# Performance work log

Hardware: AMD Instinct MI355X
Metric: run time of the kernel (lower is better)

The kernel has to match this reference:

```python
import jax, jax.numpy as jnp
import numpy as np

N_NODES = 50000
N_EDGES = 800000
D_FEAT = 64
N_OUT = 64
N_LAYERS = 2


def setup_inputs() -> dict:
    key = jax.random.key(0)
    ks = jax.random.split(key, 6)
    x = jax.random.normal(ks[0], (N_NODES, D_FEAT), dtype=jnp.float32)
    rows = jnp.sort(jax.random.randint(ks[1], (N_EDGES,), 0, N_NODES, dtype=jnp.int32))
    cols = jax.random.randint(ks[2], (N_EDGES,), 0, N_NODES, dtype=jnp.int32)
    vals = jax.random.uniform(ks[3], (N_EDGES,), dtype=jnp.float32)
    scalars = jnp.ones((N_LAYERS,), dtype=jnp.float32)  # per-layer scalar param (init ones)
    W = jax.random.normal(ks[4], (N_OUT, D_FEAT), dtype=jnp.float32) / np.sqrt(D_FEAT)
    b = jnp.zeros((N_OUT,), dtype=jnp.float32)
    return {"x": x, "rows": rows, "cols": cols, "vals": vals,
            "scalars": scalars, "W": W, "b": b}


def _spmm(rows, cols, vals, x):
    # y[r] = sum_e vals[e] * x[cols[e]]  (sparse adj in COO)
    msgs = vals[:, None] * x[cols]  # [E, D] gather + scale
    return jax.ops.segment_sum(msgs, rows, num_segments=N_NODES,
                               indices_are_sorted=True)


def reference(x, rows, cols, vals, scalars, W, b):
    # ScalarGCNNoFeatureTrans forward (dropout in eval mode = identity)
    h = x
    for l in range(N_LAYERS):
        h = jax.nn.elu(_spmm(rows, cols, vals, scalars[l] * h))
    return h @ W.T + b
```

## Files before the change

kernel.cpp:

```cpp
#include <hip/hip_runtime.h>
#include <hip/hip_fp16.h>
#include <math.h>

#define N_NODES 50000
#define N_EDGES 800000
#define D_FEAT 64
#define XCHUNKS (N_NODES * D_FEAT / 8)
#define NBLK 3125
#define ECAP 512

__device__ __forceinline__ unsigned pack2h(float a, float b) {
    __half2 h = __floats2half2_rn(a, b);
    return *reinterpret_cast<unsigned*>(&h);
}
__device__ __forceinline__ __half2 as_h2(unsigned u) {
    return *reinterpret_cast<__half2*>(&u);
}

__device__ __forceinline__ float elu_f(float x) {
    return x > 0.f ? x : (__expf(x) - 1.f);
}

__global__ __launch_bounds__(256) void prep_kernel(const int* __restrict__ rows,
                                                   const float* __restrict__ x,
                                                   int* __restrict__ row_ptr,
                                                   unsigned short* __restrict__ xhf) {
    const int i = blockIdx.x * blockDim.x + threadIdx.x;
    if (i <= N_NODES) {
        int lo = 0, hi = N_EDGES;
        while (lo < hi) {
            int mid = (lo + hi) >> 1;
            if (rows[mid] < i) lo = mid + 1; else hi = mid;
        }
        row_ptr[i] = lo;
    }
    if (i < XCHUNKS) {
        const float4 f0 = *reinterpret_cast<const float4*>(x + (size_t)i * 8);
        const float4 f1 = *reinterpret_cast<const float4*>(x + (size_t)i * 8 + 4);
        uint4 w;
        w.x = pack2h(f0.x, f0.y);
        w.y = pack2h(f0.z, f0.w);
        w.z = pack2h(f1.x, f1.y);
        w.w = pack2h(f1.z, f1.w);
        *reinterpret_cast<uint4*>(xhf + (size_t)i * 8) = w;
    }
}

template <bool MASKED>
__device__ __forceinline__ void edge_step8_lds(const char* __restrict__ hb,
                                               const int2* __restrict__ elds,
                                               int le, int le1, int boff,
                                               __half2& A0, __half2& A1,
                                               __half2& B0, __half2& B1) {
    int off[8]; unsigned v2[8];
    #pragma unroll
    for (int k = 0; k < 8; ++k) {
        const int t = le + k;
        const int idx = MASKED ? (t < le1 ? t : le1 - 1) : t;
        const int2 p = elds[idx];
        off[k] = p.x;
        v2[k]  = (unsigned)p.y;
        if (MASKED) v2[k] = (t < le1) ? v2[k] : 0u;
    }
    uint2 gg[8];
    #pragma unroll
    for (int k = 0; k < 8; ++k)
        gg[k] = *reinterpret_cast<const uint2*>(hb + (unsigned)(off[k] + boff));
    #pragma unroll
    for (int k = 0; k < 8; ++k) {
        const __half2 vv = as_h2(v2[k]);
        if (k & 1) {
            B0 = __hfma2(vv, as_h2(gg[k].x), B0);
            B1 = __hfma2(vv, as_h2(gg[k].y), B1);
        } else {
            A0 = __hfma2(vv, as_h2(gg[k].x), A0);
            A1 = __hfma2(vv, as_h2(gg[k].y), A1);
        }
    }
}

template <bool FUSE>
__global__ __launch_bounds__(256) void gcn_layer(
    const unsigned short* __restrict__ h_in,
    const int*   __restrict__ cols,
    const float* __restrict__ vals,
    const int*   __restrict__ row_ptr,
    const float* __restrict__ scalar_p,
    const float* __restrict__ W,
    const float* __restrict__ bvec,
    void*        __restrict__ h_out)
{
    __shared__ int2     elds[ECAP];
    __shared__ unsigned Wh[FUSE ? 64 * 33 : 1];
    __shared__ float    ylds[FUSE ? 4 * 4 * 68 : 1];

    const int tid  = threadIdx.x;
    const int lane = tid & 63;
    const int wave = tid >> 6;
    const int g    = lane >> 4;
    const int f4   = lane & 15;
    const int boff = f4 * 8;

    const int rb  = blockIdx.x * 16;
    const int eb0 = row_ptr[rb];
    const int eb1 = row_ptr[rb + 16];
    const int cnt = min(eb1 - eb0, ECAP);
    for (int i = tid; i < cnt; i += 256) {
        const int   c = cols[eb0 + i];
        const float v = vals[eb0 + i];
        elds[i] = make_int2(c << 7, (int)pack2h(v, v));
    }
    if constexpr (FUSE) {
        for (int i = tid; i < 64 * 32; i += 256) {
            const int j = i >> 5, c = i & 31;
            Wh[j * 33 + c] = pack2h(W[j * 64 + 2 * c], W[j * 64 + 2 * c + 1]);
        }
    }
    __syncthreads();

    const int row = rb + wave * 4 + g;
    const float s  = scalar_p[0];
    const int  e0  = row_ptr[row];
    const int  e1  = row_ptr[row + 1];
    const char* hb = (const char*)h_in;

    __half2 A0 = __floats2half2_rn(0.f, 0.f);
    __half2 A1 = A0, B0 = A0, B1 = A0;

    const int ecap = eb0 + cnt;
    const int le0 = e0 - eb0;
    const int le1 = (e1 < ecap ? e1 : ecap) - eb0;
    int le = le0;
    for (; le + 8 <= le1; le += 8)
        edge_step8_lds<false>(hb, elds, le, le1, boff, A0, A1, B0, B1);
    if (le < le1)
        edge_step8_lds<true>(hb, elds, le, le1, boff, A0, A1, B0, B1);
    for (int e = (e0 > ecap ? e0 : ecap); e < e1; ++e) {
        const int   c = cols[e];
        const float v = vals[e];
        const __half2 vv = as_h2(pack2h(v, v));
        const uint2 gg = *reinterpret_cast<const uint2*>(hb + (unsigned)((c << 7) + boff));
        A0 = __hfma2(vv, as_h2(gg.x), A0);
        A1 = __hfma2(vv, as_h2(gg.y), A1);
    }

    const float2 a0 = __half22float2(A0), a1 = __half22float2(A1);
    const float2 b0 = __half22float2(B0), b1 = __half22float2(B1);
    float4 acc;
    acc.x = elu_f((a0.x + b0.x) * s);
    acc.y = elu_f((a0.y + b0.y) * s);
    acc.z = elu_f((a1.x + b1.x) * s);
    acc.w = elu_f((a1.y + b1.y) * s);

    if constexpr (!FUSE) {
        uint2 wv;
        wv.x = pack2h(acc.x, acc.y);
        wv.y = pack2h(acc.z, acc.w);
        *reinterpret_cast<uint2*>((char*)h_out + (size_t)row * 128 + boff) = wv;
    } else {
        float* yw = ylds + wave * (4 * 68);
        *reinterpret_cast<float4*>(yw + g * 68 + f4 * 4) = acc;
        asm volatile("s_waitcnt lgkmcnt(0)" ::: "memory");

        const int j = lane;
        const float bj = bvec[j];
        float o0 = bj, o1 = bj, o2 = bj, o3 = bj;
        #pragma unroll
        for (int d0 = 0; d0 < 16; ++d0) {
            const float2 wA = __half22float2(as_h2(Wh[j * 33 + 2 * d0]));
            const float2 wB = __half22float2(as_h2(Wh[j * 33 + 2 * d0 + 1]));
            const float4 y0 = *reinterpret_cast<const float4*>(yw + 0 * 68 + d0 * 4);
            const float4 y1 = *reinterpret_cast<const float4*>(yw + 1 * 68 + d0 * 4);
            const float4 y2 = *reinterpret_cast<const float4*>(yw + 2 * 68 + d0 * 4);
            const float4 y3 = *reinterpret_cast<const float4*>(yw + 3 * 68 + d0 * 4);
            o0 = fmaf(y0.x, wA.x, o0); o0 = fmaf(y0.y, wA.y, o0);
            o0 = fmaf(y0.z, wB.x, o0); o0 = fmaf(y0.w, wB.y, o0);
            o1 = fmaf(y1.x, wA.x, o1); o1 = fmaf(y1.y, wA.y, o1);
            o1 = fmaf(y1.z, wB.x, o1); o1 = fmaf(y1.w, wB.y, o1);
            o2 = fmaf(y2.x, wA.x, o2); o2 = fmaf(y2.y, wA.y, o2);
            o2 = fmaf(y2.z, wB.x, o2); o2 = fmaf(y2.w, wB.y, o2);
            o3 = fmaf(y3.x, wA.x, o3); o3 = fmaf(y3.y, wA.y, o3);
            o3 = fmaf(y3.z, wB.x, o3); o3 = fmaf(y3.w, wB.y, o3);
        }
        const size_t rbase = (size_t)(rb + wave * 4) * D_FEAT;
        float* outp = (float*)h_out;
        outp[rbase + 0 * D_FEAT + j] = o0;
        outp[rbase + 1 * D_FEAT + j] = o1;
        outp[rbase + 2 * D_FEAT + j] = o2;
        outp[rbase + 3 * D_FEAT + j] = o3;
    }
}

extern "C" void kernel_launch(void* const* d_in, const int* in_sizes, int n_in,
                              void* d_out, int out_size, void* d_ws, size_t ws_size,
                              hipStream_t stream) {
    const float* x       = (const float*)d_in[0];
    const int*   rows    = (const int*)  d_in[1];
    const int*   cols    = (const int*)  d_in[2];
    const float* vals    = (const float*)d_in[3];
    const float* scalars = (const float*)d_in[4];
    const float* W       = (const float*)d_in[5];
    const float* b       = (const float*)d_in[6];
    float* out = (float*)d_out;

    const size_t rp_b = (sizeof(int) * (N_NODES + 1) + 255) & ~size_t(255);
    const size_t xb_b = ((size_t)N_NODES * D_FEAT * 2 + 255) & ~size_t(255);

    int*            row_ptr = (int*)d_ws;
    unsigned short* xhf     = (unsigned short*)((char*)d_ws + rp_b);
    unsigned short* h1      = (unsigned short*)((char*)d_ws + rp_b + xb_b);

    prep_kernel<<<(XCHUNKS + 255) / 256, 256, 0, stream>>>(rows, x, row_ptr, xhf);

    gcn_layer<false><<<NBLK, 256, 0, stream>>>(
        xhf, cols, vals, row_ptr, scalars + 0, nullptr, nullptr, h1);
    gcn_layer<true><<<NBLK, 256, 0, stream>>>(
        h1, cols, vals, row_ptr, scalars + 1, W, b, out);
}
```

Baseline: 48.88 us.

## Split feature table into two column halves and unfuse projection into separate kernel

Stores the fp16 node features as two 32-column half-tables, each 64 bytes per node, so each SpMM block gathers only one half. Grid size doubles, and each lane does one 4-byte gather per edge instead of 8 bytes, which shrinks the random-access working set per pass and may improve cache hit rates. The final linear projection moves out of the second layer into its own kernel. The cost is an extra launch, an extra intermediate round-trip through memory, and every block loading edge lists twice.

```diff
diff --git a/kernel.cpp b/kernel.cpp
--- a/kernel.cpp
+++ b/kernel.cpp
@@ -5,8 +5,10 @@
 #define N_NODES 50000
 #define N_EDGES 800000
 #define D_FEAT 64
-#define XCHUNKS (N_NODES * D_FEAT / 8)
-#define NBLK 3125
+#define HALF_B 64
+#define TAB_HALF_B ((size_t)N_NODES * HALF_B)
+#define XCHUNKS (N_NODES * 8)
+#define NRB 3125
 #define ECAP 512
 
 __device__ __forceinline__ unsigned pack2h(float a, float b) {
@@ -24,7 +26,7 @@
 __global__ __launch_bounds__(256) void prep_kernel(const int* __restrict__ rows,
                                                    const float* __restrict__ x,
                                                    int* __restrict__ row_ptr,
-                                                   unsigned short* __restrict__ xhf) {
+                                                   unsigned short* __restrict__ xh) {
     const int i = blockIdx.x * blockDim.x + threadIdx.x;
     if (i <= N_NODES) {
         int lo = 0, hi = N_EDGES;
@@ -35,6 +37,9 @@
         row_ptr[i] = lo;
     }
     if (i < XCHUNKS) {
+        const int node = i >> 3;
+        const int c8   = i & 7;
+        const int h    = c8 >> 2;
         const float4 f0 = *reinterpret_cast<const float4*>(x + (size_t)i * 8);
         const float4 f1 = *reinterpret_cast<const float4*>(x + (size_t)i * 8 + 4);
         uint4 w;
@@ -42,16 +47,16 @@
         w.y = pack2h(f0.z, f0.w);
         w.z = pack2h(f1.x, f1.y);
         w.w = pack2h(f1.z, f1.w);
-        *reinterpret_cast<uint4*>(xhf + (size_t)i * 8) = w;
+        char* dst = (char*)xh + (size_t)h * TAB_HALF_B + (size_t)node * HALF_B + (c8 & 3) * 16;
+        *reinterpret_cast<uint4*>(dst) = w;
     }
 }
 
 template <bool MASKED>
-__device__ __forceinline__ void edge_step8_lds(const char* __restrict__ hb,
-                                               const int2* __restrict__ elds,
-                                               int le, int le1, int boff,
-                                               __half2& A0, __half2& A1,
-                                               __half2& B0, __half2& B1) {
+__device__ __forceinline__ void edge_step8(const char* __restrict__ hb,
+                                           const int2* __restrict__ elds,
+                                           int le, int le1, int boff,
+                                           __half2& A, __half2& B) {
     int off[8]; unsigned v2[8];
     #pragma unroll
     for (int k = 0; k < 8; ++k) {
@@ -62,59 +67,46 @@
         v2[k]  = (unsigned)p.y;
         if (MASKED) v2[k] = (t < le1) ? v2[k] : 0u;
     }
-    uint2 gg[8];
+    unsigned gg[8];
     #pragma unroll
     for (int k = 0; k < 8; ++k)
-        gg[k] = *reinterpret_cast<const uint2*>(hb + (unsigned)(off[k] + boff));
+        gg[k] = *reinterpret_cast<const unsigned*>(hb + (unsigned)(off[k] + boff));
     #pragma unroll
     for (int k = 0; k < 8; ++k) {
         const __half2 vv = as_h2(v2[k]);
-        if (k & 1) {
-            B0 = __hfma2(vv, as_h2(gg[k].x), B0);
-            B1 = __hfma2(vv, as_h2(gg[k].y), B1);
-        } else {
-            A0 = __hfma2(vv, as_h2(gg[k].x), A0);
-            A1 = __hfma2(vv, as_h2(gg[k].y), A1);
-        }
-    }
-}
-
-template <bool FUSE>
-__global__ __launch_bounds__(256) void gcn_layer(
+        if (k & 1) B = __hfma2(vv, as_h2(gg[k]), B);
+        else       A = __hfma2(vv, as_h2(gg[k]), A);
+    }
+}
+
+__global__ __launch_bounds__(256) void gcn_spmm_half(
     const unsigned short* __restrict__ h_in,
     const int*   __restrict__ cols,
     const float* __restrict__ vals,
     const int*   __restrict__ row_ptr,
     const float* __restrict__ scalar_p,
-    const float* __restrict__ W,
-    const float* __restrict__ bvec,
-    void*        __restrict__ h_out)
+    unsigned short* __restrict__ h_out)
 {
-    __shared__ int2     elds[ECAP];
-    __shared__ unsigned Wh[FUSE ? 64 * 33 : 1];
-    __shared__ float    ylds[FUSE ? 4 * 4 * 68 : 1];
+    __shared__ int2 elds[ECAP];
 
     const int tid  = threadIdx.x;
     const int lane = tid & 63;
     const int wave = tid >> 6;
     const int g    = lane >> 4;
     const int f4   = lane & 15;
-    const int boff = f4 * 8;
-
-    const int rb  = blockIdx.x * 16;
+    const int boff = f4 * 4;
+
+    const int half = blockIdx.x & 1;
+    const int rb   = (blockIdx.x >> 1) * 16;
+    const char* hb = (const char*)h_in + (size_t)half * TAB_HALF_B;
+
     const int eb0 = row_ptr[rb];
     const int eb1 = row_ptr[rb + 16];
     const int cnt = min(eb1 - eb0, ECAP);
     for (int i = tid; i < cnt; i += 256) {
         const int   c = cols[eb0 + i];
         const float v = vals[eb0 + i];
-        elds[i] = make_int2(c << 7, (int)pack2h(v, v));
-    }
-    if constexpr (FUSE) {
-        for (int i = tid; i < 64 * 32; i += 256) {
-            const int j = i >> 5, c = i & 31;
-            Wh[j * 33 + c] = pack2h(W[j * 64 + 2 * c], W[j * 64 + 2 * c + 1]);
-        }
+        elds[i] = make_int2(c << 6, (int)pack2h(v, v));
     }
     __syncthreads();
 
@@ -122,73 +114,90 @@
     const float s  = scalar_p[0];
     const int  e0  = row_ptr[row];
     const int  e1  = row_ptr[row + 1];
-    const char* hb = (const char*)h_in;
-
-    __half2 A0 = __floats2half2_rn(0.f, 0.f);
-    __half2 A1 = A0, B0 = A0, B1 = A0;
+
+    __half2 A = __floats2half2_rn(0.f, 0.f);
+    __half2 B = A;
 
     const int ecap = eb0 + cnt;
     const int le0 = e0 - eb0;
     const int le1 = (e1 < ecap ? e1 : ecap) - eb0;
     int le = le0;
     for (; le + 8 <= le1; le += 8)
-        edge_step8_lds<false>(hb, elds, le, le1, boff, A0, A1, B0, B1);
+        edge_step8<false>(hb, elds, le, le1, boff, A, B);
     if (le < le1)
-        edge_step8_lds<true>(hb, elds, le, le1, boff, A0, A1, B0, B1);
+        edge_step8<true>(hb, elds, le, le1, boff, A, B);
     for (int e = (e0 > ecap ? e0 : ecap); e < e1; ++e) {
         const int   c = cols[e];
         const float v = vals[e];
-        const __half2 vv = as_h2(pack2h(v, v));
-        const uint2 gg = *reinterpret_cast<const uint2*>(hb + (unsigned)((c << 7) + boff));
-        A0 = __hfma2(vv, as_h2(gg.x), A0);
-        A1 = __hfma2(vv, as_h2(gg.y), A1);
-    }
-
-    const float2 a0 = __half22float2(A0), a1 = __half22float2(A1);
-    const float2 b0 = __half22float2(B0), b1 = __half22float2(B1);
-    float4 acc;
-    acc.x = elu_f((a0.x + b0.x) * s);
-    acc.y = elu_f((a0.y + b0.y) * s);
-    acc.z = elu_f((a1.x + b1.x) * s);
-    acc.w = elu_f((a1.y + b1.y) * s);
-
-    if constexpr (!FUSE) {
-        uint2 wv;
-        wv.x = pack2h(acc.x, acc.y);
-        wv.y = pack2h(acc.z, acc.w);
-        *reinterpret_cast<uint2*>((char*)h_out + (size_t)row * 128 + boff) = wv;
-    } else {
-        float* yw = ylds + wave * (4 * 68);
-        *reinterpret_cast<float4*>(yw + g * 68 + f4 * 4) = acc;
-        asm volatile("s_waitcnt lgkmcnt(0)" ::: "memory");
-
-        const int j = lane;
-        const float bj = bvec[j];
-        float o0 = bj, o1 = bj, o2 = bj, o3 = bj;
-        #pragma unroll
-        for (int d0 = 0; d0 < 16; ++d0) {
-            const float2 wA = __half22float2(as_h2(Wh[j * 33 + 2 * d0]));
-            const float2 wB = __half22float2(as_h2(Wh[j * 33 + 2 * d0 + 1]));
-            const float4 y0 = *reinterpret_cast<const float4*>(yw + 0 * 68 + d0 * 4);
-            const float4 y1 = *reinterpret_cast<const float4*>(yw + 1 * 68 + d0 * 4);
-            const float4 y2 = *reinterpret_cast<const float4*>(yw + 2 * 68 + d0 * 4);
-            const float4 y3 = *reinterpret_cast<const float4*>(yw + 3 * 68 + d0 * 4);
-            o0 = fmaf(y0.x, wA.x, o0); o0 = fmaf(y0.y, wA.y, o0);
-            o0 = fmaf(y0.z, wB.x, o0); o0 = fmaf(y0.w, wB.y, o0);
-            o1 = fmaf(y1.x, wA.x, o1); o1 = fmaf(y1.y, wA.y, o1);
-            o1 = fmaf(y1.z, wB.x, o1); o1 = fmaf(y1.w, wB.y, o1);
-            o2 = fmaf(y2.x, wA.x, o2); o2 = fmaf(y2.y, wA.y, o2);
-            o2 = fmaf(y2.z, wB.x, o2); o2 = fmaf(y2.w, wB.y, o2);
-            o3 = fmaf(y3.x, wA.x, o3); o3 = fmaf(y3.y, wA.y, o3);
-            o3 = fmaf(y3.z, wB.x, o3); o3 = fmaf(y3.w, wB.y, o3);
-        }
-        const size_t rbase = (size_t)(rb + wave * 4) * D_FEAT;
-        float* outp = (float*)h_out;
-        outp[rbase + 0 * D_FEAT + j] = o0;
-        outp[rbase + 1 * D_FEAT + j] = o1;
-        outp[rbase + 2 * D_FEAT + j] = o2;
-        outp[rbase + 3 * D_FEAT + j] = o3;
-    }
+        const unsigned gg = *reinterpret_cast<const unsigned*>(hb + (unsigned)((c << 6) + boff));
+        A = __hfma2(as_h2(pack2h(v, v)), as_h2(gg), A);
+    }
+
+    const float2 a = __half22float2(A);
+    const float2 bb = __half22float2(B);
+    const float rx = elu_f((a.x + bb.x) * s);
+    const float ry = elu_f((a.y + bb.y) * s);
+
+    char* dst = (char*)h_out + (size_t)half * TAB_HALF_B + (size_t)row * HALF_B + boff;
+    *reinterpret_cast<unsigned*>(dst) = pack2h(rx, ry);
+}
+
+__global__ __launch_bounds__(256) void proj_kernel(
+    const unsigned short* __restrict__ y,
+    const float* __restrict__ W,
+    const float* __restrict__ bvec,
+    float*       __restrict__ out)
+{
+    __shared__ unsigned Wh[64 * 33];
+    __shared__ float    ylds[4 * 4 * 68];
+
+    const int tid  = threadIdx.x;
+    const int lane = tid & 63;
+    const int wave = tid >> 6;
+    const int g    = lane >> 4;
+    const int f4   = lane & 15;
+
+    for (int i = tid; i < 64 * 32; i += 256) {
+        const int j = i >> 5, c = i & 31;
+        Wh[j * 33 + c] = pack2h(W[j * 64 + 2 * c], W[j * 64 + 2 * c + 1]);
+    }
+
+    const int rb  = blockIdx.x * 16;
+    const int row = rb + wave * 4 + g;
+    const char* src = (const char*)y + (f4 < 8 ? (size_t)0 : TAB_HALF_B)
+                    + (size_t)row * HALF_B + (f4 & 7) * 8;
+    const uint2 yy = *reinterpret_cast<const uint2*>(src);
+    const float2 p0 = __half22float2(as_h2(yy.x));
+    const float2 p1 = __half22float2(as_h2(yy.y));
+    float* yw = ylds + wave * (4 * 68);
+    *reinterpret_cast<float4*>(yw + g * 68 + f4 * 4) = make_float4(p0.x, p0.y, p1.x, p1.y);
+    __syncthreads();
+
+    const int j = lane;
+    const float bj = bvec[j];
+    float o0 = bj, o1 = bj, o2 = bj, o3 = bj;
+    #pragma unroll
+    for (int d0 = 0; d0 < 16; ++d0) {
+        const float2 wA = __half22float2(as_h2(Wh[j * 33 + 2 * d0]));
+        const float2 wB = __half22float2(as_h2(Wh[j * 33 + 2 * d0 + 1]));
+        const float4 y0 = *reinterpret_cast<const float4*>(yw + 0 * 68 + d0 * 4);
+        const float4 y1 = *reinterpret_cast<const float4*>(yw + 1 * 68 + d0 * 4);
+        const float4 y2 = *reinterpret_cast<const float4*>(yw + 2 * 68 + d0 * 4);
+        const float4 y3 = *reinterpret_cast<const float4*>(yw + 3 * 68 + d0 * 4);
+        o0 = fmaf(y0.x, wA.x, o0); o0 = fmaf(y0.y, wA.y, o0);
+        o0 = fmaf(y0.z, wB.x, o0); o0 = fmaf(y0.w, wB.y, o0);
+        o1 = fmaf(y1.x, wA.x, o1); o1 = fmaf(y1.y, wA.y, o1);
+        o1 = fmaf(y1.z, wB.x, o1); o1 = fmaf(y1.w, wB.y, o1);
+        o2 = fmaf(y2.x, wA.x, o2); o2 = fmaf(y2.y, wA.y, o2);
+        o2 = fmaf(y2.z, wB.x, o2); o2 = fmaf(y2.w, wB.y, o2);
+        o3 = fmaf(y3.x, wA.x, o3); o3 = fmaf(y3.y, wA.y, o3);
+        o3 = fmaf(y3.z, wB.x, o3); o3 = fmaf(y3.w, wB.y, o3);
+    }
+    const size_t rbase = (size_t)(rb + wave * 4) * D_FEAT;
+    out[rbase + 0 * D_FEAT + j] = o0;
+    out[rbase + 1 * D_FEAT + j] = o1;
+    out[rbase + 2 * D_FEAT + j] = o2;
+    out[rbase + 3 * D_FEAT + j] = o3;
 }
 
 extern "C" void kernel_launch(void* const* d_in, const int* in_sizes, int n_in,
@@ -204,16 +213,17 @@
     float* out = (float*)d_out;
 
     const size_t rp_b = (sizeof(int) * (N_NODES + 1) + 255) & ~size_t(255);
-    const size_t xb_b = ((size_t)N_NODES * D_FEAT * 2 + 255) & ~size_t(255);
+    const size_t tb_b = (2 * TAB_HALF_B + 255) & ~size_t(255);
 
     int*            row_ptr = (int*)d_ws;
-    unsigned short* xhf     = (unsigned short*)((char*)d_ws + rp_b);
-    unsigned short* h1      = (unsigned short*)((char*)d_ws + rp_b + xb_b);
-
-    prep_kernel<<<(XCHUNKS + 255) / 256, 256, 0, stream>>>(rows, x, row_ptr, xhf);
-
-    gcn_layer<false><<<NBLK, 256, 0, stream>>>(
-        xhf, cols, vals, row_ptr, scalars + 0, nullptr, nullptr, h1);
-    gcn_layer<true><<<NBLK, 256, 0, stream>>>(
-        h1, cols, vals, row_ptr, scalars + 1, W, b, out);
-}
+    unsigned short* xh      = (unsigned short*)((char*)d_ws + rp_b);
+    unsigned short* h1      = (unsigned short*)((char*)d_ws + rp_b + tb_b);
+    unsigned short* yv      = (unsigned short*)((char*)d_ws + rp_b + 2 * tb_b);
+
+    prep_kernel<<<(XCHUNKS + 255) / 256, 256, 0, stream>>>(rows, x, row_ptr, xh);
+
+    gcn_spmm_half<<<2 * NRB, 256, 0, stream>>>(xh, cols, vals, row_ptr, scalars + 0, h1);
+    gcn_spmm_half<<<2 * NRB, 256, 0, stream>>>(h1, cols, vals, row_ptr, scalars + 1, yv);
+
+    proj_kernel<<<NRB, 256, 0, stream>>>(yv, W, b, out);
+}
```

New measurement: 57.76 us. 18.2% more time.

## Process 32 rows per block with 8 lanes per row using 16-byte gathers

Applied to the files above, without the earlier changes.

Each block now covers 32 rows instead of 16, and 8 lanes share a row, each gathering 16 bytes (8 halves) per edge instead of 8 bytes. This halves the number of gather instructions per edge and widens each memory access. The edge staging buffer grows to 768 entries and the fused projection works on 8 rows per wave using a half-precision LDS staging buffer. In exchange, each row has fewer lanes, so per-row latency hiding and occupancy may drop, and the grid shrinks to about 1563 blocks.

```diff
diff --git a/kernel.cpp b/kernel.cpp
--- a/kernel.cpp
+++ b/kernel.cpp
@@ -6,8 +6,9 @@
 #define N_EDGES 800000
 #define D_FEAT 64
 #define XCHUNKS (N_NODES * D_FEAT / 8)
-#define NBLK 3125
-#define ECAP 512
+#define RPB 32
+#define NBLK ((N_NODES + RPB - 1) / RPB)
+#define ECAP 768
 
 __device__ __forceinline__ unsigned pack2h(float a, float b) {
     __half2 h = __floats2half2_rn(a, b);
@@ -47,14 +48,16 @@
 }
 
 template <bool MASKED>
-__device__ __forceinline__ void edge_step8_lds(const char* __restrict__ hb,
+__device__ __forceinline__ void edge_step4_lds(const char* __restrict__ hb,
                                                const int2* __restrict__ elds,
                                                int le, int le1, int boff,
                                                __half2& A0, __half2& A1,
-                                               __half2& B0, __half2& B1) {
-    int off[8]; unsigned v2[8];
+                                               __half2& A2, __half2& A3,
+                                               __half2& B0, __half2& B1,
+                                               __half2& B2, __half2& B3) {
+    int off[4]; unsigned v2[4];
     #pragma unroll
-    for (int k = 0; k < 8; ++k) {
+    for (int k = 0; k < 4; ++k) {
         const int t = le + k;
         const int idx = MASKED ? (t < le1 ? t : le1 - 1) : t;
         const int2 p = elds[idx];
@@ -62,19 +65,23 @@
         v2[k]  = (unsigned)p.y;
         if (MASKED) v2[k] = (t < le1) ? v2[k] : 0u;
     }
-    uint2 gg[8];
+    uint4 gg[4];
     #pragma unroll
-    for (int k = 0; k < 8; ++k)
-        gg[k] = *reinterpret_cast<const uint2*>(hb + (unsigned)(off[k] + boff));
+    for (int k = 0; k < 4; ++k)
+        gg[k] = *reinterpret_cast<const uint4*>(hb + (unsigned)(off[k] + boff));
     #pragma unroll
-    for (int k = 0; k < 8; ++k) {
+    for (int k = 0; k < 4; ++k) {
         const __half2 vv = as_h2(v2[k]);
         if (k & 1) {
             B0 = __hfma2(vv, as_h2(gg[k].x), B0);
             B1 = __hfma2(vv, as_h2(gg[k].y), B1);
+            B2 = __hfma2(vv, as_h2(gg[k].z), B2);
+            B3 = __hfma2(vv, as_h2(gg[k].w), B3);
         } else {
             A0 = __hfma2(vv, as_h2(gg[k].x), A0);
             A1 = __hfma2(vv, as_h2(gg[k].y), A1);
+            A2 = __hfma2(vv, as_h2(gg[k].z), A2);
+            A3 = __hfma2(vv, as_h2(gg[k].w), A3);
         }
     }
 }
@@ -92,18 +99,19 @@
 {
     __shared__ int2     elds[ECAP];
     __shared__ unsigned Wh[FUSE ? 64 * 33 : 1];
-    __shared__ float    ylds[FUSE ? 4 * 4 * 68 : 1];
+    __shared__ char     ylds[FUSE ? 4 * 8 * 136 : 1];
 
     const int tid  = threadIdx.x;
     const int lane = tid & 63;
     const int wave = tid >> 6;
-    const int g    = lane >> 4;
-    const int f4   = lane & 15;
-    const int boff = f4 * 8;
-
-    const int rb  = blockIdx.x * 16;
+    const int g    = lane >> 3;
+    const int l8   = lane & 7;
+    const int boff = l8 * 16;
+
+    const int rb  = blockIdx.x * RPB;
+    const int rtop = (rb + RPB < N_NODES) ? rb + RPB : N_NODES;
     const int eb0 = row_ptr[rb];
-    const int eb1 = row_ptr[rb + 16];
+    const int eb1 = row_ptr[rtop];
     const int cnt = min(eb1 - eb0, ECAP);
     for (int i = tid; i < cnt; i += 256) {
         const int   c = cols[eb0 + i];
@@ -118,76 +126,83 @@
     }
     __syncthreads();
 
-    const int row = rb + wave * 4 + g;
+    const int row = rb + wave * 8 + g;
     const float s  = scalar_p[0];
-    const int  e0  = row_ptr[row];
-    const int  e1  = row_ptr[row + 1];
+    int e0 = 0, e1 = 0;
+    if (row < N_NODES) { e0 = row_ptr[row]; e1 = row_ptr[row + 1]; }
     const char* hb = (const char*)h_in;
 
     __half2 A0 = __floats2half2_rn(0.f, 0.f);
-    __half2 A1 = A0, B0 = A0, B1 = A0;
+    __half2 A1 = A0, A2 = A0, A3 = A0, B0 = A0, B1 = A0, B2 = A0, B3 = A0;
 
     const int ecap = eb0 + cnt;
     const int le0 = e0 - eb0;
     const int le1 = (e1 < ecap ? e1 : ecap) - eb0;
     int le = le0;
-    for (; le + 8 <= le1; le += 8)
-        edge_step8_lds<false>(hb, elds, le, le1, boff, A0, A1, B0, B1);
+    for (; le + 4 <= le1; le += 4)
+        edge_step4_lds<false>(hb, elds, le, le1, boff, A0, A1, A2, A3, B0, B1, B2, B3);
     if (le < le1)
-        edge_step8_lds<true>(hb, elds, le, le1, boff, A0, A1, B0, B1);
+        edge_step4_lds<true>(hb, elds, le, le1, boff, A0, A1, A2, A3, B0, B1, B2, B3);
     for (int e = (e0 > ecap ? e0 : ecap); e < e1; ++e) {
         const int   c = cols[e];
         const float v = vals[e];
         const __half2 vv = as_h2(pack2h(v, v));
-        const uint2 gg = *reinterpret_cast<const uint2*>(hb + (unsigned)((c << 7) + boff));
+        const uint4 gg = *reinterpret_cast<const uint4*>(hb + (unsigned)((c << 7) + boff));
         A0 = __hfma2(vv, as_h2(gg.x), A0);
         A1 = __hfma2(vv, as_h2(gg.y), A1);
-    }
-
-    const float2 a0 = __half22float2(A0), a1 = __half22float2(A1);
-    const float2 b0 = __half22float2(B0), b1 = __half22float2(B1);
-    float4 acc;
-    acc.x = elu_f((a0.x + b0.x) * s);
-    acc.y = elu_f((a0.y + b0.y) * s);
-    acc.z = elu_f((a1.x + b1.x) * s);
-    acc.w = elu_f((a1.y + b1.y) * s);
+        A2 = __hfma2(vv, as_h2(gg.z), A2);
+        A3 = __hfma2(vv, as_h2(gg.w), A3);
+    }
+
+    float r[8];
+    {
+        const float2 p0 = __half22float2(A0), q0 = __half22float2(B0);
+        const float2 p1 = __half22float2(A1), q1 = __half22float2(B1);
+        const float2 p2 = __half22float2(A2), q2 = __half22float2(B2);
+        const float2 p3 = __half22float2(A3), q3 = __half22float2(B3);
+        r[0] = elu_f((p0.x + q0.x) * s); r[1] = elu_f((p0.y + q0.y) * s);
+        r[2] = elu_f((p1.x + q1.x) * s); r[3] = elu_f((p1.y + q1.y) * s);
+        r[4] = elu_f((p2.x + q2.x) * s); r[5] = elu_f((p2.y + q2.y) * s);
+        r[6] = elu_f((p3.x + q3.x) * s); r[7] = elu_f((p3.y + q3.y) * s);
+    }
+    uint4 packed;
+    packed.x = pack2h(r[0], r[1]);
+    packed.y = pack2h(r[2], r[3]);
+    packed.z = pack2h(r[4], r[5]);
+    packed.w = pack2h(r[6], r[7]);
 
     if constexpr (!FUSE) {
-        uint2 wv;
-        wv.x = pack2h(acc.x, acc.y);
-        wv.y = pack2h(acc.z, acc.w);
-        *reinterpret_cast<uint2*>((char*)h_out + (size_t)row * 128 + boff) = wv;
+        if (row < N_NODES)
+            *reinterpret_cast<uint4*>((char*)h_out + (size_t)row * 128 + boff) = packed;
     } else {
-        float* yw = ylds + wave * (4 * 68);
-        *reinterpret_cast<float4*>(yw + g * 68 + f4 * 4) = acc;
+        char* yw = ylds + wave * (8 * 136);
+        *reinterpret_cast<uint4*>(yw + g * 136 + l8 * 16) = packed;
         asm volatile("s_waitcnt lgkmcnt(0)" ::: "memory");
 
         const int j = lane;
         const float bj = bvec[j];
-        float o0 = bj, o1 = bj, o2 = bj, o3 = bj;
+        float o[8];
+        #pragma unroll
+        for (int q = 0; q < 8; ++q) o[q] = bj;
         #pragma unroll
         for (int d0 = 0; d0 < 16; ++d0) {
             const float2 wA = __half22float2(as_h2(Wh[j * 33 + 2 * d0]));
             const float2 wB = __half22float2(as_h2(Wh[j * 33 + 2 * d0 + 1]));
-            const float4 y0 = *reinterpret_cast<const float4*>(yw + 0 * 68 + d0 * 4);
-            const float4 y1 = *reinterpret_cast<const float4*>(yw + 1 * 68 + d0 * 4);
-            const float4 y2 = *reinterpret_cast<const float4*>(yw + 2 * 68 + d0 * 4);
-            const float4 y3 = *reinterpret_cast<const float4*>(yw + 3 * 68 + d0 * 4);
-            o0 = fmaf(y0.x, wA.x, o0); o0 = fmaf(y0.y, wA.y, o0);
-            o0 = fmaf(y0.z, wB.x, o0); o0 = fmaf(y0.w, wB.y, o0);
-            o1 = fmaf(y1.x, wA.x, o1); o1 = fmaf(y1.y, wA.y, o1);
-            o1 = fmaf(y1.z, wB.x, o1); o1 = fmaf(y1.w, wB.y, o1);
-            o2 = fmaf(y2.x, wA.x, o2); o2 = fmaf(y2.y, wA.y, o2);
-            o2 = fmaf(y2.z, wB.x, o2); o2 = fmaf(y2.w, wB.y, o2);
-            o3 = fmaf(y3.x, wA.x, o3); o3 = fmaf(y3.y, wA.y, o3);
-            o3 = fmaf(y3.z, wB.x, o3); o3 = fmaf(y3.w, wB.y, o3);
-        }
-        const size_t rbase = (size_t)(rb + wave * 4) * D_FEAT;
+            #pragma unroll
+            for (int q = 0; q < 8; ++q) {
+                const uint2 yy = *reinterpret_cast<const uint2*>(yw + q * 136 + d0 * 8);
+                const float2 p0 = __half22float2(as_h2(yy.x));
+                const float2 p1 = __half22float2(as_h2(yy.y));
+                o[q] = fmaf(p0.x, wA.x, o[q]); o[q] = fmaf(p0.y, wA.y, o[q]);
+                o[q] = fmaf(p1.x, wB.x, o[q]); o[q] = fmaf(p1.y, wB.y, o[q]);
+            }
+        }
+        const int rbase = rb + wave * 8;
         float* outp = (float*)h_out;
-        outp[rbase + 0 * D_FEAT + j] = o0;
-        outp[rbase + 1 * D_FEAT + j] = o1;
-        outp[rbase + 2 * D_FEAT + j] = o2;
-        outp[rbase + 3 * D_FEAT + j] = o3;
+        #pragma unroll
+        for (int q = 0; q < 8; ++q)
+            if (rbase + q < N_NODES)
+                outp[(size_t)(rbase + q) * D_FEAT + j] = o[q];
     }
 }
 
```

Result: slower. 85.44 us (+74.8%).
